# Kernel optimization log

Hardware: AMD Instinct MI355X
Metric: run time of the kernel (lower is better)

The kernel has to match this reference:

```python
import jax, jax.numpy as jnp
import numpy as np

B, S, H, NH = 4, 320, 512, 8
DH = H // NH
RAND_S = 320  # weibo randomAttention size
NEG = -1e15


def setup_inputs() -> dict:
    rng = jax.random.key(0)
    ks = jax.random.split(rng, 14)
    s = 0.02
    return {
        "query": jax.random.normal(ks[0], (B, S, H), jnp.float32),
        "key": jax.random.normal(ks[1], (B, S, H), jnp.float32),
        "value": jax.random.normal(ks[2], (B, S, H), jnp.float32),
        "rel_pos_embedding": jax.random.normal(ks[3], (B, S, S, H), jnp.float32),
        "seq_len": jax.random.randint(ks[4], (B,), 1, S + 1),
        "lex_num": 0,
        "Wq": jax.random.normal(ks[5], (H, H), jnp.float32) * s,
        "bq": jax.random.normal(ks[6], (H,), jnp.float32) * s,
        "Wv": jax.random.normal(ks[7], (H, H), jnp.float32) * s,
        "bv": jax.random.normal(ks[8], (H,), jnp.float32) * s,
        "Wr": jax.random.normal(ks[9], (H, H), jnp.float32) * s,
        "br": jax.random.normal(ks[10], (H,), jnp.float32) * s,
        "u": jax.random.normal(ks[11], (NH, DH), jnp.float32) * s,
        "v": jax.random.normal(ks[12], (NH, DH), jnp.float32) * s,
        "rand_attn": jax.random.normal(ks[13], (1, NH, RAND_S, RAND_S), jnp.float32) * s,
    }


def reference(query, key, value, rel_pos_embedding, seq_len, lex_num,
              Wq, bq, Wv, bv, Wr, br, u, v, rand_attn):
    # Linear projections (torch Linear: x @ W.T + b). Note: key is NOT projected.
    q = query @ Wq.T + bq                      # [B,S,H]
    val = value @ Wv.T + bv                    # [B,S,H]
    rel = rel_pos_embedding @ Wr.T + br        # [B,S,S,H]

    # Split heads
    q = q.reshape(B, S, NH, DH).transpose(0, 2, 1, 3)     # [B,NH,S,DH]
    k = key.reshape(B, S, NH, DH).transpose(0, 2, 1, 3)   # [B,NH,S,DH]
    val = val.reshape(B, S, NH, DH).transpose(0, 2, 1, 3) # [B,NH,S,DH]
    rel = rel.reshape(B, S, S, NH, DH)                    # [B,Sq,Sk,NH,DH]

    # A+C: (q + u) k^T
    A_C = jnp.einsum('bhqd,bhkd->bhqk', q + u[None, :, None, :], k)
    # B+D: (q + v) contracted with relative position embeddings
    B_D = jnp.einsum('bhqd,bqkhd->bhqk', q + v[None, :, None, :], rel)

    scores = A_C + B_D + rand_attn[:, :, :S, :S]          # [B,NH,S,S]

    lengths = seq_len + lex_num                           # [B]
    mask = jnp.arange(S)[None, :] < lengths[:, None]      # [B,S] key mask
    scores = jnp.where(mask[:, None, None, :], scores, NEG)

    attn = jax.nn.softmax(scores, axis=-1)                # dropout p=0 -> identity
    out = jnp.einsum('bhqk,bhkd->bhqd', attn, val)        # [B,NH,S,DH]
    return out.transpose(0, 2, 1, 3).reshape(B, S, H)
```

## Files before the change

kernel.cpp:

```cpp
#include <hip/hip_runtime.h>


#define NEGV (-1e15f)

typedef unsigned int u32;

__device__ __forceinline__ void gl_lds16(const float* g, float* l) {
  __builtin_amdgcn_global_load_lds(
      (const __attribute__((address_space(1))) u32*)(g),
      (__attribute__((address_space(3))) u32*)(l), 16, 0, 0);
}

__device__ __forceinline__ float dot4f(const float4 a, const float4 b) {
  return a.x*b.x + a.y*b.y + a.z*b.z + a.w*b.w;
}

__global__ __launch_bounds__(256) void k1_proj(
    const float* __restrict__ query, const float* __restrict__ value,
    const float* __restrict__ Wq, const float* __restrict__ bq,
    const float* __restrict__ Wv, const float* __restrict__ bv,
    const float* __restrict__ u, const float* __restrict__ v,
    float* __restrict__ qu, float* __restrict__ qv, float* __restrict__ valp)
{
  const int rt = blockIdx.x;
  const int ct = blockIdx.y;
  const int which = blockIdx.z;
  const int t = threadIdx.x;
  const int R0 = rt * 16;

  __shared__ float xs[16][516];

  const float* X = which ? value : query;
  const float* W = which ? Wv : Wq;
  const float* bias = which ? bv : bq;

  #pragma unroll
  for (int j = 0; j < 8; ++j) {
    int f4 = t + 256 * j;
    int row = f4 >> 7, c4 = f4 & 127;
    float4 xv = *reinterpret_cast<const float4*>(X + (size_t)(R0 + row) * 512 + c4 * 4);
    *reinterpret_cast<float4*>(&xs[row][c4 * 4]) = xv;
  }
  __syncthreads();

  const int r = t >> 4, clo = t & 15;
  #pragma unroll
  for (int sub = 0; sub < 2; ++sub) {
    const int cb = ct * 128 + sub * 64 + clo * 4;
    float a0 = 0.f, a1 = 0.f, a2 = 0.f, a3 = 0.f;
    const float* w0p = W + (size_t)(cb + 0) * 512;
    const float* w1p = W + (size_t)(cb + 1) * 512;
    const float* w2p = W + (size_t)(cb + 2) * 512;
    const float* w3p = W + (size_t)(cb + 3) * 512;
    #pragma unroll 2
    for (int m4 = 0; m4 < 128; ++m4) {
      float4 x4 = *reinterpret_cast<const float4*>(&xs[r][m4 * 4]);
      float4 w0 = *reinterpret_cast<const float4*>(w0p + m4 * 4);
      float4 w1 = *reinterpret_cast<const float4*>(w1p + m4 * 4);
      float4 w2 = *reinterpret_cast<const float4*>(w2p + m4 * 4);
      float4 w3 = *reinterpret_cast<const float4*>(w3p + m4 * 4);
      a0 += dot4f(x4, w0);
      a1 += dot4f(x4, w1);
      a2 += dot4f(x4, w2);
      a3 += dot4f(x4, w3);
    }
    a0 += bias[cb + 0]; a1 += bias[cb + 1]; a2 += bias[cb + 2]; a3 += bias[cb + 3];
    const size_t ob = (size_t)(R0 + r) * 512 + cb;
    if (which == 0) {
      float4 o1, o2;
      o1.x = a0 + u[cb + 0]; o1.y = a1 + u[cb + 1]; o1.z = a2 + u[cb + 2]; o1.w = a3 + u[cb + 3];
      o2.x = a0 + v[cb + 0]; o2.y = a1 + v[cb + 1]; o2.z = a2 + v[cb + 2]; o2.w = a3 + v[cb + 3];
      *reinterpret_cast<float4*>(qu + ob) = o1;
      *reinterpret_cast<float4*>(qv + ob) = o2;
    } else {
      float4 o; o.x = a0; o.y = a1; o.z = a2; o.w = a3;
      *reinterpret_cast<float4*>(valp + ob) = o;
    }
  }
}

__global__ __launch_bounds__(256) void k2_w(
    const float* __restrict__ qv, const float* __restrict__ Wr, const float* __restrict__ br,
    float* __restrict__ w_ws, float* __restrict__ c_ws)
{
  const int rt = blockIdx.x;
  const int h  = blockIdx.y;
  const int t = threadIdx.x;
  const int R0 = rt * 16;

  __shared__ float qs[16][68];
  {
    int row = t >> 4, d4 = t & 15;
    float4 x = *reinterpret_cast<const float4*>(qv + (size_t)(R0 + row) * 512 + h * 64 + d4 * 4);
    *reinterpret_cast<float4*>(&qs[row][d4 * 4]) = x;
  }
  __syncthreads();

  const int r = t >> 4, clo = t & 15;
  #pragma unroll
  for (int sub = 0; sub < 8; ++sub) {
    const int eb = sub * 64 + clo * 4;
    float4 acc; acc.x = 0.f; acc.y = 0.f; acc.z = 0.f; acc.w = 0.f;
    #pragma unroll 4
    for (int d = 0; d < 64; ++d) {
      float s = qs[r][d];
      float4 w4 = *reinterpret_cast<const float4*>(Wr + (size_t)(h * 64 + d) * 512 + eb);
      acc.x += s * w4.x; acc.y += s * w4.y; acc.z += s * w4.z; acc.w += s * w4.w;
    }
    *reinterpret_cast<float4*>(w_ws + (size_t)(R0 + r) * 4096 + h * 512 + eb) = acc;
  }
  if (t < 16) {
    float cs = 0.f;
    for (int d = 0; d < 64; ++d) cs += qs[t][d] * br[h * 64 + d];
    c_ws[(size_t)(R0 + t) * 8 + h] = cs;
  }
}

__global__ __launch_bounds__(320) void k3_ac(
    const float* __restrict__ qu, const float* __restrict__ key,
    const float* __restrict__ rand_attn, const float* __restrict__ c_ws,
    float* __restrict__ sc_ws)
{
  const int qt = blockIdx.x;
  const int h  = blockIdx.y;
  const int b  = blockIdx.z;
  const int t  = threadIdx.x;
  const int q0 = qt * 16;

  const float* kr = key + ((size_t)b * 320 + t) * 512 + h * 64;
  float4 krow[16];
  #pragma unroll
  for (int i = 0; i < 16; ++i) krow[i] = *reinterpret_cast<const float4*>(kr + i * 4);

  float acc[16];
  #pragma unroll
  for (int qi = 0; qi < 16; ++qi) {
    const float* qrow = qu + ((size_t)b * 320 + q0 + qi) * 512 + h * 64;
    float a = 0.f;
    #pragma unroll
    for (int i = 0; i < 16; ++i) {
      float4 q4 = *reinterpret_cast<const float4*>(qrow + i * 4);
      a += dot4f(q4, krow[i]);
    }
    acc[qi] = a;
  }
  #pragma unroll
  for (int qi = 0; qi < 16; ++qi) {
    const int q = q0 + qi;
    float r = rand_attn[((size_t)h * 320 + q) * 320 + t];
    float c = c_ws[((size_t)b * 320 + q) * 8 + h];
    sc_ws[(((size_t)b * 320 + q) * 8 + h) * 320 + t] = acc[qi] + r + c;
  }
}

__global__ __launch_bounds__(256, 2) void k4_attn(
    const float* __restrict__ rpe,
    const int* __restrict__ seq_len, const int* __restrict__ lex_num,
    const float* __restrict__ w_ws, const float* __restrict__ sc_ws,
    const float* __restrict__ valp,
    float* __restrict__ out)
{
  const int q = blockIdx.x;
  const int b = blockIdx.y;
  const int t = threadIdx.x;
  const int w = t >> 6;
  const int lane = t & 63;
  const int row8 = lane >> 3;
  const int chunk = lane & 7;
  const int rc = (row8 ^ chunk) & 7;

  __shared__ float bufA[2][16][512];
  __shared__ float sc[8][320];

  const size_t bq = (size_t)b * 320 + q;
  const float* rpe_bq = rpe + bq * 320 * 512;

  int g[8];
  #pragma unroll
  for (int j = 0; j < 8; ++j) {
    int o = (w * 8 + j) * 1024 + lane * 16;
    int row = o >> 11;
    int ch  = (o >> 8) & 7;
    int win = (o >> 7) & 1;
    int slot = (o >> 4) & 7;
    int i = win * 8 + (slot ^ ((row ^ ch) & 7));
    g[j] = row * 512 + (ch * 16 + i) * 4;
  }

  #pragma unroll
  for (int j = 0; j < 8; ++j)
    gl_lds16(rpe_bq + g[j], &bufA[0][0][0] + (w * 8 + j) * 256);

  const int h0 = 2 * w, h1 = 2 * w + 1;
  const float* wb0 = w_ws + bq * 4096 + (size_t)h0 * 512 + chunk * 64;
  const float* wb1 = w_ws + bq * 4096 + (size_t)h1 * 512 + chunk * 64;
  float4 wc0[16], wc1[16];
  #pragma unroll
  for (int i = 0; i < 16; ++i) {
    wc0[i] = *reinterpret_cast<const float4*>(wb0 + i * 4);
    wc1[i] = *reinterpret_cast<const float4*>(wb1 + i * 4);
  }

  const int len = seq_len[b] + lex_num[0];
  const float* scb = sc_ws + bq * 8 * 320;
  for (int h = 0; h < 8; ++h) {
    for (int k = t; k < 320; k += 256) {
      float vv = scb[h * 320 + k];
      sc[h][k] = (k < len) ? vv : NEGV;
    }
  }
  __syncthreads();

  const int Cb0 = row8 * 2048 + chunk * 256 + rc * 16;
  const char* bufbase = reinterpret_cast<const char*>(&bufA[0][0][0]);

  int cb = 0;
  for (int tile = 0; tile < 20; ++tile) {
    if (tile + 1 < 20) {
      const float* src = rpe_bq + (size_t)(tile + 1) * 8192;
      float* dst = &bufA[cb ^ 1][0][0];
      #pragma unroll
      for (int j = 0; j < 8; ++j)
        gl_lds16(src + g[j], dst + (w * 8 + j) * 256);
    }

    const char* bufc = bufbase + cb * 32768;
    #pragma unroll
    for (int pass = 0; pass < 2; ++pass) {
      const int C = Cb0 + pass * 16384;
      float a0 = 0.f, a1 = 0.f;
      #pragma unroll
      for (int i = 0; i < 16; ++i) {
        const float4 r4 = *reinterpret_cast<const float4*>(bufc + (C ^ (i << 4)));
        a0 += dot4f(r4, wc0[i]);
        a1 += dot4f(r4, wc1[i]);
      }
      a0 += __shfl_xor(a0, 1, 8);
      a0 += __shfl_xor(a0, 2, 8);
      a0 += __shfl_xor(a0, 4, 8);
      a1 += __shfl_xor(a1, 1, 8);
      a1 += __shfl_xor(a1, 2, 8);
      a1 += __shfl_xor(a1, 4, 8);
      if (chunk == 0) {
        const int kk = tile * 16 + pass * 8 + row8;
        sc[h0][kk] += a0;
        sc[h1][kk] += a1;
      }
    }
    __syncthreads();
    cb ^= 1;
  }

  {
    const int h = t >> 5, m = t & 31;
    float vals[10];
    float mx = -3.0e38f;
    #pragma unroll
    for (int i = 0; i < 10; ++i) { vals[i] = sc[h][m + 32 * i]; mx = fmaxf(mx, vals[i]); }
    mx = fmaxf(mx, __shfl_xor(mx, 1, 32));
    mx = fmaxf(mx, __shfl_xor(mx, 2, 32));
    mx = fmaxf(mx, __shfl_xor(mx, 4, 32));
    mx = fmaxf(mx, __shfl_xor(mx, 8, 32));
    mx = fmaxf(mx, __shfl_xor(mx, 16, 32));
    float s = 0.f;
    #pragma unroll
    for (int i = 0; i < 10; ++i) { vals[i] = __expf(vals[i] - mx); s += vals[i]; }
    s += __shfl_xor(s, 1, 32);
    s += __shfl_xor(s, 2, 32);
    s += __shfl_xor(s, 4, 32);
    s += __shfl_xor(s, 8, 32);
    s += __shfl_xor(s, 16, 32);
    const float inv = 1.0f / s;
    #pragma unroll
    for (int i = 0; i < 10; ++i) sc[h][m + 32 * i] = vals[i] * inv;
  }
  __syncthreads();

  {
    const int h = t >> 5, d2 = t & 31;
    float2 a0; a0.x = 0.f; a0.y = 0.f;
    float2 a1; a1.x = 0.f; a1.y = 0.f;
    const float* vb = valp + (size_t)b * 320 * 512 + h * 64 + d2 * 2;
    #pragma unroll 4
    for (int k = 0; k < 320; k += 2) {
      float p0 = sc[h][k], p1 = sc[h][k + 1];
      float2 v0 = *reinterpret_cast<const float2*>(vb + (size_t)k * 512);
      float2 v1 = *reinterpret_cast<const float2*>(vb + (size_t)(k + 1) * 512);
      a0.x += p0 * v0.x; a0.y += p0 * v0.y;
      a1.x += p1 * v1.x; a1.y += p1 * v1.y;
    }
    float2 o; o.x = a0.x + a1.x; o.y = a0.y + a1.y;
    *reinterpret_cast<float2*>(out + bq * 512 + h * 64 + d2 * 2) = o;
  }
}

extern "C" void kernel_launch(void* const* d_in, const int* in_sizes, int n_in,
                              void* d_out, int out_size, void* d_ws, size_t ws_size,
                              hipStream_t stream) {
  const float* query = (const float*)d_in[0];
  const float* key   = (const float*)d_in[1];
  const float* value = (const float*)d_in[2];
  const float* rpe   = (const float*)d_in[3];
  const int*   seq_len = (const int*)d_in[4];
  const int*   lex_num = (const int*)d_in[5];
  const float* Wq = (const float*)d_in[6];
  const float* bq = (const float*)d_in[7];
  const float* Wv = (const float*)d_in[8];
  const float* bv = (const float*)d_in[9];
  const float* Wr = (const float*)d_in[10];
  const float* br = (const float*)d_in[11];
  const float* u  = (const float*)d_in[12];
  const float* v  = (const float*)d_in[13];
  const float* rnd = (const float*)d_in[14];

  float* out = (float*)d_out;
  float* ws = (float*)d_ws;
  float* qu    = ws;
  float* qv    = ws + 655360;
  float* valp  = ws + 1310720;
  float* w_ws  = ws + 1966080;
  float* c_ws  = ws + 7208960;
  float* sc_ws = ws + 7219200;

  k1_proj<<<dim3(80, 4, 2), 256, 0, stream>>>(query, value, Wq, bq, Wv, bv, u, v, qu, qv, valp);
  k2_w<<<dim3(80, 8), 256, 0, stream>>>(qv, Wr, br, w_ws, c_ws);
  k3_ac<<<dim3(20, 8, 4), 320, 0, stream>>>(qu, key, rnd, c_ws, sc_ws);
  k4_attn<<<dim3(320, 4), 256, 0, stream>>>(rpe, seq_len, lex_num, w_ws, sc_ws, valp, out);
}
```

Before: 688.6 us.

## Fuse Wr-folding and q·k score computation into the attention kernel

Removes the separate k2_w and k3_ac kernels. Each attention block now computes its own per-query Wr-folded weights into the idle second LDS buffer, plus the bias term and the masked A+C scores with rand_attn, directly in shared memory. This drops the large w_ws and sc_ws workspace round-trips and two launches, and skips q·k dot products for masked keys. In exchange the per-block prologue does more serial global reads of Wr and key before the rpe streaming loop, which may lengthen the prologue and is only partly hidden behind the first tile prefetch.

```diff
diff --git a/kernel.cpp b/kernel.cpp
--- a/kernel.cpp
+++ b/kernel.cpp
@@ -79,84 +79,12 @@
   }
 }
 
-__global__ __launch_bounds__(256) void k2_w(
-    const float* __restrict__ qv, const float* __restrict__ Wr, const float* __restrict__ br,
-    float* __restrict__ w_ws, float* __restrict__ c_ws)
-{
-  const int rt = blockIdx.x;
-  const int h  = blockIdx.y;
-  const int t = threadIdx.x;
-  const int R0 = rt * 16;
-
-  __shared__ float qs[16][68];
-  {
-    int row = t >> 4, d4 = t & 15;
-    float4 x = *reinterpret_cast<const float4*>(qv + (size_t)(R0 + row) * 512 + h * 64 + d4 * 4);
-    *reinterpret_cast<float4*>(&qs[row][d4 * 4]) = x;
-  }
-  __syncthreads();
-
-  const int r = t >> 4, clo = t & 15;
-  #pragma unroll
-  for (int sub = 0; sub < 8; ++sub) {
-    const int eb = sub * 64 + clo * 4;
-    float4 acc; acc.x = 0.f; acc.y = 0.f; acc.z = 0.f; acc.w = 0.f;
-    #pragma unroll 4
-    for (int d = 0; d < 64; ++d) {
-      float s = qs[r][d];
-      float4 w4 = *reinterpret_cast<const float4*>(Wr + (size_t)(h * 64 + d) * 512 + eb);
-      acc.x += s * w4.x; acc.y += s * w4.y; acc.z += s * w4.z; acc.w += s * w4.w;
-    }
-    *reinterpret_cast<float4*>(w_ws + (size_t)(R0 + r) * 4096 + h * 512 + eb) = acc;
-  }
-  if (t < 16) {
-    float cs = 0.f;
-    for (int d = 0; d < 64; ++d) cs += qs[t][d] * br[h * 64 + d];
-    c_ws[(size_t)(R0 + t) * 8 + h] = cs;
-  }
-}
-
-__global__ __launch_bounds__(320) void k3_ac(
-    const float* __restrict__ qu, const float* __restrict__ key,
-    const float* __restrict__ rand_attn, const float* __restrict__ c_ws,
-    float* __restrict__ sc_ws)
-{
-  const int qt = blockIdx.x;
-  const int h  = blockIdx.y;
-  const int b  = blockIdx.z;
-  const int t  = threadIdx.x;
-  const int q0 = qt * 16;
-
-  const float* kr = key + ((size_t)b * 320 + t) * 512 + h * 64;
-  float4 krow[16];
-  #pragma unroll
-  for (int i = 0; i < 16; ++i) krow[i] = *reinterpret_cast<const float4*>(kr + i * 4);
-
-  float acc[16];
-  #pragma unroll
-  for (int qi = 0; qi < 16; ++qi) {
-    const float* qrow = qu + ((size_t)b * 320 + q0 + qi) * 512 + h * 64;
-    float a = 0.f;
-    #pragma unroll
-    for (int i = 0; i < 16; ++i) {
-      float4 q4 = *reinterpret_cast<const float4*>(qrow + i * 4);
-      a += dot4f(q4, krow[i]);
-    }
-    acc[qi] = a;
-  }
-  #pragma unroll
-  for (int qi = 0; qi < 16; ++qi) {
-    const int q = q0 + qi;
-    float r = rand_attn[((size_t)h * 320 + q) * 320 + t];
-    float c = c_ws[((size_t)b * 320 + q) * 8 + h];
-    sc_ws[(((size_t)b * 320 + q) * 8 + h) * 320 + t] = acc[qi] + r + c;
-  }
-}
-
 __global__ __launch_bounds__(256, 2) void k4_attn(
-    const float* __restrict__ rpe,
+    const float* __restrict__ rpe, const float* __restrict__ key,
+    const float* __restrict__ Wr, const float* __restrict__ br,
+    const float* __restrict__ rand_attn,
     const int* __restrict__ seq_len, const int* __restrict__ lex_num,
-    const float* __restrict__ w_ws, const float* __restrict__ sc_ws,
+    const float* __restrict__ qu, const float* __restrict__ qv,
     const float* __restrict__ valp,
     float* __restrict__ out)
 {
@@ -167,13 +95,13 @@
   const int lane = t & 63;
   const int row8 = lane >> 3;
   const int chunk = lane & 7;
-  const int rc = (row8 ^ chunk) & 7;
 
   __shared__ float bufA[2][16][512];
   __shared__ float sc[8][320];
 
   const size_t bq = (size_t)b * 320 + q;
   const float* rpe_bq = rpe + bq * 320 * 512;
+  float* wscr = &bufA[1][0][0];
 
   int g[8];
   #pragma unroll
@@ -191,26 +119,68 @@
   for (int j = 0; j < 8; ++j)
     gl_lds16(rpe_bq + g[j], &bufA[0][0][0] + (w * 8 + j) * 256);
 
+  const int hh = t >> 5, m = t & 31;
+  const float* qv_row = qv + bq * 512 + hh * 64;
+
+  {
+    float4 a4[4];
+    #pragma unroll
+    for (int ii = 0; ii < 4; ++ii) { a4[ii].x = 0.f; a4[ii].y = 0.f; a4[ii].z = 0.f; a4[ii].w = 0.f; }
+    const float* wrb = Wr + (size_t)(hh * 64) * 512 + m * 16;
+    #pragma unroll 4
+    for (int d = 0; d < 64; ++d) {
+      float s = qv_row[d];
+      const float4* w4 = reinterpret_cast<const float4*>(wrb + (size_t)d * 512);
+      #pragma unroll
+      for (int ii = 0; ii < 4; ++ii) {
+        a4[ii].x += s * w4[ii].x; a4[ii].y += s * w4[ii].y;
+        a4[ii].z += s * w4[ii].z; a4[ii].w += s * w4[ii].w;
+      }
+    }
+    #pragma unroll
+    for (int ii = 0; ii < 4; ++ii)
+      *reinterpret_cast<float4*>(wscr + hh * 512 + m * 16 + ii * 4) = a4[ii];
+  }
+
+  float c = 0.f;
+  #pragma unroll 8
+  for (int d = 0; d < 64; ++d) c += qv_row[d] * br[hh * 64 + d];
+
+  const int len = seq_len[b] + lex_num[0];
+  {
+    const float* qup = qu + bq * 512 + hh * 64;
+    const float* keyb = key + (size_t)b * 320 * 512 + hh * 64;
+    const float* rnd_hq = rand_attn + ((size_t)hh * 320 + q) * 320;
+    #pragma unroll
+    for (int i = 0; i < 10; ++i) {
+      const int k = m + 32 * i;
+      float val;
+      if (k < len) {
+        const float* kr = keyb + (size_t)k * 512;
+        float a = 0.f;
+        #pragma unroll
+        for (int ii = 0; ii < 16; ++ii)
+          a += dot4f(reinterpret_cast<const float4*>(qup)[ii],
+                     reinterpret_cast<const float4*>(kr)[ii]);
+        val = a + rnd_hq[k] + c;
+      } else {
+        val = NEGV;
+      }
+      sc[hh][k] = val;
+    }
+  }
+  __syncthreads();
+
   const int h0 = 2 * w, h1 = 2 * w + 1;
-  const float* wb0 = w_ws + bq * 4096 + (size_t)h0 * 512 + chunk * 64;
-  const float* wb1 = w_ws + bq * 4096 + (size_t)h1 * 512 + chunk * 64;
   float4 wc0[16], wc1[16];
   #pragma unroll
   for (int i = 0; i < 16; ++i) {
-    wc0[i] = *reinterpret_cast<const float4*>(wb0 + i * 4);
-    wc1[i] = *reinterpret_cast<const float4*>(wb1 + i * 4);
-  }
-
-  const int len = seq_len[b] + lex_num[0];
-  const float* scb = sc_ws + bq * 8 * 320;
-  for (int h = 0; h < 8; ++h) {
-    for (int k = t; k < 320; k += 256) {
-      float vv = scb[h * 320 + k];
-      sc[h][k] = (k < len) ? vv : NEGV;
-    }
-  }
-  __syncthreads();
-
+    wc0[i] = *reinterpret_cast<const float4*>(wscr + h0 * 512 + chunk * 64 + i * 4);
+    wc1[i] = *reinterpret_cast<const float4*>(wscr + h1 * 512 + chunk * 64 + i * 4);
+  }
+  __syncthreads();
+
+  const int rc = (row8 ^ chunk) & 7;
   const int Cb0 = row8 * 2048 + chunk * 256 + rc * 16;
   const char* bufbase = reinterpret_cast<const char*>(&bufA[0][0][0]);
 
@@ -252,11 +222,10 @@
   }
 
   {
-    const int h = t >> 5, m = t & 31;
     float vals[10];
     float mx = -3.0e38f;
     #pragma unroll
-    for (int i = 0; i < 10; ++i) { vals[i] = sc[h][m + 32 * i]; mx = fmaxf(mx, vals[i]); }
+    for (int i = 0; i < 10; ++i) { vals[i] = sc[hh][m + 32 * i]; mx = fmaxf(mx, vals[i]); }
     mx = fmaxf(mx, __shfl_xor(mx, 1, 32));
     mx = fmaxf(mx, __shfl_xor(mx, 2, 32));
     mx = fmaxf(mx, __shfl_xor(mx, 4, 32));
@@ -272,25 +241,25 @@
     s += __shfl_xor(s, 16, 32);
     const float inv = 1.0f / s;
     #pragma unroll
-    for (int i = 0; i < 10; ++i) sc[h][m + 32 * i] = vals[i] * inv;
-  }
-  __syncthreads();
-
-  {
-    const int h = t >> 5, d2 = t & 31;
+    for (int i = 0; i < 10; ++i) sc[hh][m + 32 * i] = vals[i] * inv;
+  }
+  __syncthreads();
+
+  {
+    const int d2 = m;
     float2 a0; a0.x = 0.f; a0.y = 0.f;
     float2 a1; a1.x = 0.f; a1.y = 0.f;
-    const float* vb = valp + (size_t)b * 320 * 512 + h * 64 + d2 * 2;
+    const float* vb = valp + (size_t)b * 320 * 512 + hh * 64 + d2 * 2;
     #pragma unroll 4
     for (int k = 0; k < 320; k += 2) {
-      float p0 = sc[h][k], p1 = sc[h][k + 1];
+      float p0 = sc[hh][k], p1 = sc[hh][k + 1];
       float2 v0 = *reinterpret_cast<const float2*>(vb + (size_t)k * 512);
       float2 v1 = *reinterpret_cast<const float2*>(vb + (size_t)(k + 1) * 512);
       a0.x += p0 * v0.x; a0.y += p0 * v0.y;
       a1.x += p1 * v1.x; a1.y += p1 * v1.y;
     }
     float2 o; o.x = a0.x + a1.x; o.y = a0.y + a1.y;
-    *reinterpret_cast<float2*>(out + bq * 512 + h * 64 + d2 * 2) = o;
+    *reinterpret_cast<float2*>(out + bq * 512 + hh * 64 + d2 * 2) = o;
   }
 }
 
@@ -318,12 +287,7 @@
   float* qu    = ws;
   float* qv    = ws + 655360;
   float* valp  = ws + 1310720;
-  float* w_ws  = ws + 1966080;
-  float* c_ws  = ws + 7208960;
-  float* sc_ws = ws + 7219200;
 
   k1_proj<<<dim3(80, 4, 2), 256, 0, stream>>>(query, value, Wq, bq, Wv, bv, u, v, qu, qv, valp);
-  k2_w<<<dim3(80, 8), 256, 0, stream>>>(qv, Wr, br, w_ws, c_ws);
-  k3_ac<<<dim3(20, 8, 4), 320, 0, stream>>>(qu, key, rnd, c_ws, sc_ws);
-  k4_attn<<<dim3(320, 4), 256, 0, stream>>>(rpe, seq_len, lex_num, w_ws, sc_ws, valp, out);
-}
+  k4_attn<<<dim3(320, 4), 256, 0, stream>>>(rpe, key, Wr, br, rnd, seq_len, lex_num, qu, qv, valp, out);
+}
```

New measurement: 684.5 us. Within noise of the previous version (-0.6%).
